# Optimization experiments

Hardware: AMD Instinct MI355X
Metric: run time of the kernel (lower is better)

Reference implementation:

```python
import jax, jax.numpy as jnp
import numpy as np

EPS = 1e-6

def setup_inputs() -> dict:
    key = jax.random.key(0)
    k1, k2 = jax.random.split(key)
    S, B, H, F = 2048, 4, 2048, 8192
    x = jax.random.normal(k1, (S, B, H), dtype=jnp.float32)
    scale = jnp.ones((H,), dtype=jnp.float32)
    ln_bias = jnp.zeros((H,), dtype=jnp.float32)
    kernel = jax.random.normal(k2, (H, F), dtype=jnp.float32) * 0.02  # ~variance_scaling fan_in
    return {"x": x, "scale": scale, "ln_bias": ln_bias, "kernel": kernel}

def reference(x, scale, ln_bias, kernel):
    # LayerNorm over last (hidden) axis, stats in fp32
    mu = jnp.mean(x, axis=-1, keepdims=True)
    var = jnp.mean(jnp.square(x - mu), axis=-1, keepdims=True)
    y = (x - mu) * jax.lax.rsqrt(var + EPS) * scale + ln_bias  # [S,B,H]
    # Dense: contract hidden axis against kernel [H,F]
    z = jnp.einsum('sbh,hf->sbf', y, kernel)  # [S,B,F]
    # return_layernorm_output=True -> (dense_out, ln_out)
    return (z, y)
```

## Files before the change

### kernel.cpp

```cpp
#include <hip/hip_runtime.h>
#include <stdint.h>


typedef __attribute__((ext_vector_type(8))) short short8;
typedef __attribute__((ext_vector_type(4))) float floatx4;

__device__ __forceinline__ unsigned short f2bf(float f) {
    unsigned u = __builtin_bit_cast(unsigned, f);
    u += 0x7fffu + ((u >> 16) & 1u);
    return (unsigned short)(u >> 16);
}

__global__ __launch_bounds__(256) void ln_kernel(
    const float* __restrict__ x, const float* __restrict__ scale,
    const float* __restrict__ bias, float* __restrict__ y,
    unsigned short* __restrict__ ybf, int H)
{
    const int row = blockIdx.x;
    const float* xr = x + (size_t)row * H;
    const int tid = threadIdx.x;

    float4 v0 = ((const float4*)xr)[tid];
    float4 v1 = ((const float4*)xr)[tid + 256];

    float s  = v0.x + v0.y + v0.z + v0.w + v1.x + v1.y + v1.z + v1.w;
    float ss = v0.x*v0.x + v0.y*v0.y + v0.z*v0.z + v0.w*v0.w
             + v1.x*v1.x + v1.y*v1.y + v1.z*v1.z + v1.w*v1.w;

    #pragma unroll
    for (int off = 32; off > 0; off >>= 1) {
        s  += __shfl_down(s,  off, 64);
        ss += __shfl_down(ss, off, 64);
    }
    __shared__ float rs[4], rq[4];
    if ((tid & 63) == 0) { rs[tid >> 6] = s; rq[tid >> 6] = ss; }
    __syncthreads();
    float ts = rs[0] + rs[1] + rs[2] + rs[3];
    float tq = rq[0] + rq[1] + rq[2] + rq[3];
    float mean = ts / (float)H;
    float var  = tq / (float)H - mean * mean;
    float rstd = rsqrtf(var + 1e-6f);

    float4 sc0 = ((const float4*)scale)[tid];
    float4 sc1 = ((const float4*)scale)[tid + 256];
    float4 b0  = ((const float4*)bias)[tid];
    float4 b1  = ((const float4*)bias)[tid + 256];

    float4 o0, o1;
    o0.x = (v0.x - mean) * rstd * sc0.x + b0.x;
    o0.y = (v0.y - mean) * rstd * sc0.y + b0.y;
    o0.z = (v0.z - mean) * rstd * sc0.z + b0.z;
    o0.w = (v0.w - mean) * rstd * sc0.w + b0.w;
    o1.x = (v1.x - mean) * rstd * sc1.x + b1.x;
    o1.y = (v1.y - mean) * rstd * sc1.y + b1.y;
    o1.z = (v1.z - mean) * rstd * sc1.z + b1.z;
    o1.w = (v1.w - mean) * rstd * sc1.w + b1.w;

    float* yr = y + (size_t)row * H;
    ((float4*)yr)[tid]       = o0;
    ((float4*)yr)[tid + 256] = o1;

    unsigned short* br = ybf + (size_t)row * H;
    uint2 p0, p1;
    p0.x = (unsigned)f2bf(o0.x) | ((unsigned)f2bf(o0.y) << 16);
    p0.y = (unsigned)f2bf(o0.z) | ((unsigned)f2bf(o0.w) << 16);
    p1.x = (unsigned)f2bf(o1.x) | ((unsigned)f2bf(o1.y) << 16);
    p1.y = (unsigned)f2bf(o1.z) | ((unsigned)f2bf(o1.w) << 16);
    ((uint2*)br)[tid]       = p0;
    ((uint2*)br)[tid + 256] = p1;
}

__global__ __launch_bounds__(256) void transpose_cast_kernel(
    const float* __restrict__ W, unsigned short* __restrict__ Bt,
    int K, int F)
{
    __shared__ float tile[64][65];
    const int kBase = blockIdx.y * 64;
    const int fBase = blockIdx.x * 64;
    const int tid = threadIdx.x;

    #pragma unroll
    for (int p = 0; p < 4; ++p) {
        int kl = (tid >> 4) + p * 16;
        int fl = (tid & 15) * 4;
        float4 v = *(const float4*)&W[(size_t)(kBase + kl) * F + fBase + fl];
        tile[kl][fl]     = v.x;
        tile[kl][fl + 1] = v.y;
        tile[kl][fl + 2] = v.z;
        tile[kl][fl + 3] = v.w;
    }
    __syncthreads();

    #pragma unroll
    for (int p = 0; p < 2; ++p) {
        int fl = (tid >> 3) + p * 32;
        int k8 = (tid & 7) * 8;
        unsigned w[4];
        #pragma unroll
        for (int j = 0; j < 4; ++j) {
            unsigned lo = f2bf(tile[k8 + 2*j][fl]);
            unsigned hi = f2bf(tile[k8 + 2*j + 1][fl]);
            w[j] = lo | (hi << 16);
        }
        uint4 out = make_uint4(w[0], w[1], w[2], w[3]);
        *(uint4*)&Bt[(size_t)(fBase + fl) * K + kBase + k8] = out;
    }
}

#define BM 128
#define BN 128
#define BK 32

__global__ __launch_bounds__(256) void gemm_bf16_bt(
    const unsigned short* __restrict__ A,
    const unsigned short* __restrict__ Bt,
    float* __restrict__ C,
    int M, int N, int K)
{
    __shared__ unsigned short lsA[BM * BK];
    __shared__ unsigned short lsB[BN * BK];

    const int tid   = threadIdx.x;
    const int lane  = tid & 63;
    const int wave  = tid >> 6;
    const int waveM = wave >> 1;
    const int waveN = wave & 1;
    const int quad  = lane >> 4;
    const int l16   = lane & 15;
    const int qswz  = (quad ^ ((l16 >> 1) & 3)) * 8;

    const int bm = blockIdx.y * BM;
    const int bn = blockIdx.x * BN;

    const unsigned short* gA = A  + (size_t)bm * K;
    const unsigned short* gB = Bt + (size_t)bn * K;

    floatx4 acc[4][4] = {};

    for (int k0 = 0; k0 < K; k0 += BK) {
        __syncthreads();
        #pragma unroll
        for (int i = 0; i < 2; ++i) {
            int e   = i * 256 + tid;
            int row = e >> 2;
            int cs  = (e & 3) ^ ((row >> 1) & 3);
            __builtin_amdgcn_global_load_lds(
                (const __attribute__((address_space(1))) unsigned int*)
                    (gA + (size_t)row * K + k0 + cs * 8),
                (__attribute__((address_space(3))) unsigned int*)
                    (lsA + (size_t)e * 8),
                16, 0, 0);
        }
        #pragma unroll
        for (int i = 0; i < 2; ++i) {
            int e   = i * 256 + tid;
            int row = e >> 2;
            int cs  = (e & 3) ^ ((row >> 1) & 3);
            __builtin_amdgcn_global_load_lds(
                (const __attribute__((address_space(1))) unsigned int*)
                    (gB + (size_t)row * K + k0 + cs * 8),
                (__attribute__((address_space(3))) unsigned int*)
                    (lsB + (size_t)e * 8),
                16, 0, 0);
        }
        __syncthreads();

        short8 a[4], b[4];
        #pragma unroll
        for (int mi = 0; mi < 4; ++mi)
            a[mi] = *(const short8*)&lsA[(waveM*64 + mi*16 + l16) * BK + qswz];
        #pragma unroll
        for (int ni = 0; ni < 4; ++ni)
            b[ni] = *(const short8*)&lsB[(waveN*64 + ni*16 + l16) * BK + qswz];

        #pragma unroll
        for (int mi = 0; mi < 4; ++mi)
            #pragma unroll
            for (int ni = 0; ni < 4; ++ni)
                acc[mi][ni] = __builtin_amdgcn_mfma_f32_16x16x32_bf16(
                    a[mi], b[ni], acc[mi][ni], 0, 0, 0);
    }

    #pragma unroll
    for (int mi = 0; mi < 4; ++mi) {
        #pragma unroll
        for (int ni = 0; ni < 4; ++ni) {
            int col = bn + waveN*64 + ni*16 + l16;
            #pragma unroll
            for (int r = 0; r < 4; ++r) {
                int row = bm + waveM*64 + mi*16 + quad*4 + r;
                C[(size_t)row * N + col] = acc[mi][ni][r];
            }
        }
    }
}

extern "C" void kernel_launch(void* const* d_in, const int* in_sizes, int n_in,
                              void* d_out, int out_size, void* d_ws, size_t ws_size,
                              hipStream_t stream) {
    const float* x      = (const float*)d_in[0];
    const float* scale  = (const float*)d_in[1];
    const float* lnbias = (const float*)d_in[2];
    const float* W      = (const float*)d_in[3];

    const int H = in_sizes[1];
    const int M = in_sizes[0] / H;
    const int F = in_sizes[3] / H;

    float* z = (float*)d_out;
    float* y = z + (size_t)M * F;

    unsigned short* Abf = (unsigned short*)d_ws;
    unsigned short* Btb = Abf + (size_t)M * H;

    ln_kernel<<<M, 256, 0, stream>>>(x, scale, lnbias, y, Abf, H);
    transpose_cast_kernel<<<dim3(F / 64, H / 64), 256, 0, stream>>>(W, Btb, H, F);
    gemm_bf16_bt<<<dim3(F / BN, M / BM), 256, 0, stream>>>(Abf, Btb, z, M, F, H);
}
```

Baseline: 740.8 us.

## Rewrite GEMM with 256x256 tiles, 8 waves, double-buffered LDS and XCD remap

Replaces the 128x128 single-buffered GEMM with a 256x256-tile, 512-thread kernel. It double-buffers LDS in half-K stages so global-to-LDS loads overlap MFMA work, using partial vmcnt waits and raw barriers. It also remaps workgroups across the 8 XCDs for L2 locality and raises MFMA wave priority. This targets low arithmetic intensity and exposed load latency, at the cost of more LDS (128KB per block) and more registers per thread.

```diff
diff --git a/kernel.cpp b/kernel.cpp
--- a/kernel.cpp
+++ b/kernel.cpp
@@ -107,89 +107,140 @@
     }
 }
 
-#define BM 128
-#define BN 128
-#define BK 32
-
-__global__ __launch_bounds__(256) void gemm_bf16_bt(
+#define GBM 256
+#define GBN 256
+#define GBK 64
+
+__device__ __forceinline__ void stage_half(
+    const unsigned short* __restrict__ gA,
+    const unsigned short* __restrict__ gB,
+    unsigned short* dstA,
+    unsigned short* dstB,
+    int t, int kh, int K, int tid)
+{
+    const size_t kb = (size_t)t * GBK + (size_t)kh * 32;
+    #pragma unroll
+    for (int i = 0; i < 2; ++i) {
+        int e  = i * 512 + tid;
+        int r  = e >> 2;
+        int c2 = (e & 3) ^ ((r >> 2) & 3);
+        __builtin_amdgcn_global_load_lds(
+            (const __attribute__((address_space(1))) unsigned int*)
+                (gA + (size_t)r * K + kb + c2 * 8),
+            (__attribute__((address_space(3))) unsigned int*)(dstA + e * 8),
+            16, 0, 0);
+    }
+    #pragma unroll
+    for (int i = 0; i < 2; ++i) {
+        int e  = i * 512 + tid;
+        int r  = e >> 2;
+        int c2 = (e & 3) ^ ((r >> 2) & 3);
+        __builtin_amdgcn_global_load_lds(
+            (const __attribute__((address_space(1))) unsigned int*)
+                (gB + (size_t)r * K + kb + c2 * 8),
+            (__attribute__((address_space(3))) unsigned int*)(dstB + e * 8),
+            16, 0, 0);
+    }
+}
+
+__device__ __forceinline__ void compute_phase(
+    const unsigned short* bufA,
+    const unsigned short* bufB,
+    floatx4 (&acc)[8][4],
+    int waveM, int waveN, int quad, int l16, int sl)
+{
+    short8 a[8], b[4];
+    #pragma unroll
+    for (int mi = 0; mi < 8; ++mi) {
+        int r = waveM * 128 + mi * 16 + l16;
+        a[mi] = *(const short8*)(bufA + ((size_t)r * 4 + sl) * 8);
+    }
+    #pragma unroll
+    for (int ni = 0; ni < 4; ++ni) {
+        int r = waveN * 64 + ni * 16 + l16;
+        b[ni] = *(const short8*)(bufB + ((size_t)r * 4 + sl) * 8);
+    }
+    __builtin_amdgcn_s_setprio(1);
+    #pragma unroll
+    for (int mi = 0; mi < 8; ++mi)
+        #pragma unroll
+        for (int ni = 0; ni < 4; ++ni)
+            acc[mi][ni] = __builtin_amdgcn_mfma_f32_16x16x32_bf16(
+                a[mi], b[ni], acc[mi][ni], 0, 0, 0);
+    __builtin_amdgcn_s_setprio(0);
+}
+
+__global__ __launch_bounds__(512, 2) void gemm_bf16_8w(
     const unsigned short* __restrict__ A,
     const unsigned short* __restrict__ Bt,
     float* __restrict__ C,
     int M, int N, int K)
 {
-    __shared__ unsigned short lsA[BM * BK];
-    __shared__ unsigned short lsB[BN * BK];
+    __shared__ __align__(128) unsigned short lds[2][2][2][8192];
 
     const int tid   = threadIdx.x;
     const int lane  = tid & 63;
     const int wave  = tid >> 6;
-    const int waveM = wave >> 1;
-    const int waveN = wave & 1;
+    const int waveM = wave >> 2;
+    const int waveN = wave & 3;
     const int quad  = lane >> 4;
     const int l16   = lane & 15;
-    const int qswz  = (quad ^ ((l16 >> 1) & 3)) * 8;
-
-    const int bm = blockIdx.y * BM;
-    const int bn = blockIdx.x * BN;
-
-    const unsigned short* gA = A  + (size_t)bm * K;
-    const unsigned short* gB = Bt + (size_t)bn * K;
-
-    floatx4 acc[4][4] = {};
-
-    for (int k0 = 0; k0 < K; k0 += BK) {
-        __syncthreads();
-        #pragma unroll
-        for (int i = 0; i < 2; ++i) {
-            int e   = i * 256 + tid;
-            int row = e >> 2;
-            int cs  = (e & 3) ^ ((row >> 1) & 3);
-            __builtin_amdgcn_global_load_lds(
-                (const __attribute__((address_space(1))) unsigned int*)
-                    (gA + (size_t)row * K + k0 + cs * 8),
-                (__attribute__((address_space(3))) unsigned int*)
-                    (lsA + (size_t)e * 8),
-                16, 0, 0);
-        }
-        #pragma unroll
-        for (int i = 0; i < 2; ++i) {
-            int e   = i * 256 + tid;
-            int row = e >> 2;
-            int cs  = (e & 3) ^ ((row >> 1) & 3);
-            __builtin_amdgcn_global_load_lds(
-                (const __attribute__((address_space(1))) unsigned int*)
-                    (gB + (size_t)row * K + k0 + cs * 8),
-                (__attribute__((address_space(3))) unsigned int*)
-                    (lsB + (size_t)e * 8),
-                16, 0, 0);
-        }
-        __syncthreads();
-
-        short8 a[4], b[4];
-        #pragma unroll
-        for (int mi = 0; mi < 4; ++mi)
-            a[mi] = *(const short8*)&lsA[(waveM*64 + mi*16 + l16) * BK + qswz];
-        #pragma unroll
-        for (int ni = 0; ni < 4; ++ni)
-            b[ni] = *(const short8*)&lsB[(waveN*64 + ni*16 + l16) * BK + qswz];
-
-        #pragma unroll
-        for (int mi = 0; mi < 4; ++mi)
-            #pragma unroll
-            for (int ni = 0; ni < 4; ++ni)
-                acc[mi][ni] = __builtin_amdgcn_mfma_f32_16x16x32_bf16(
-                    a[mi], b[ni], acc[mi][ni], 0, 0, 0);
-    }
-
-    #pragma unroll
-    for (int mi = 0; mi < 4; ++mi) {
+    const int sl    = quad ^ (l16 >> 2);
+
+    const int nwg = gridDim.x;
+    const int cpx = nwg >> 3;
+    const int bid = blockIdx.x;
+    const int wg  = (bid & 7) * cpx + (bid >> 3);
+    const int tilesN = N >> 8;
+    const int tm = wg / tilesN;
+    const int tn = wg % tilesN;
+
+    const unsigned short* gA = A  + (size_t)tm * GBM * K;
+    const unsigned short* gB = Bt + (size_t)tn * GBN * K;
+
+    const int NTt = K >> 6;
+
+    floatx4 acc[8][4] = {};
+
+    stage_half(gA, gB, &lds[0][0][0][0], &lds[0][1][0][0], 0, 0, K, tid);
+    stage_half(gA, gB, &lds[0][0][1][0], &lds[0][1][1][0], 0, 1, K, tid);
+    stage_half(gA, gB, &lds[1][0][0][0], &lds[1][1][0][0], 1, 0, K, tid);
+    asm volatile("s_waitcnt vmcnt(8)" ::: "memory");
+    __builtin_amdgcn_s_barrier();
+
+    for (int t = 0; t < NTt; ++t) {
+        const int p = t & 1;
+        {
+            int ts = (t + 1 < NTt) ? (t + 1) : (NTt - 1);
+            stage_half(gA, gB, &lds[p ^ 1][0][1][0], &lds[p ^ 1][1][1][0],
+                       ts, 1, K, tid);
+            compute_phase(&lds[p][0][0][0], &lds[p][1][0][0], acc,
+                          waveM, waveN, quad, l16, sl);
+            asm volatile("s_waitcnt vmcnt(8)" ::: "memory");
+            __builtin_amdgcn_s_barrier();
+        }
+        {
+            int ts = (t + 2 < NTt) ? (t + 2) : (NTt - 1);
+            stage_half(gA, gB, &lds[p][0][0][0], &lds[p][1][0][0],
+                       ts, 0, K, tid);
+            compute_phase(&lds[p][0][1][0], &lds[p][1][1][0], acc,
+                          waveM, waveN, quad, l16, sl);
+            asm volatile("s_waitcnt vmcnt(8)" ::: "memory");
+            __builtin_amdgcn_s_barrier();
+        }
+    }
+
+    const size_t bm = (size_t)tm * GBM;
+    const size_t bn = (size_t)tn * GBN;
+    #pragma unroll
+    for (int mi = 0; mi < 8; ++mi) {
         #pragma unroll
         for (int ni = 0; ni < 4; ++ni) {
-            int col = bn + waveN*64 + ni*16 + l16;
+            size_t col = bn + (size_t)waveN * 64 + ni * 16 + l16;
             #pragma unroll
             for (int r = 0; r < 4; ++r) {
-                int row = bm + waveM*64 + mi*16 + quad*4 + r;
-                C[(size_t)row * N + col] = acc[mi][ni][r];
+                size_t row = bm + (size_t)waveM * 128 + mi * 16 + quad * 4 + r;
+                C[row * N + col] = acc[mi][ni][r];
             }
         }
     }
@@ -215,5 +266,5 @@
 
     ln_kernel<<<M, 256, 0, stream>>>(x, scale, lnbias, y, Abf, H);
     transpose_cast_kernel<<<dim3(F / 64, H / 64), 256, 0, stream>>>(W, Btb, H, F);
-    gemm_bf16_bt<<<dim3(F / BN, M / BM), 256, 0, stream>>>(Abf, Btb, z, M, F, H);
-}
+    gemm_bf16_8w<<<dim3((M / GBM) * (F / GBN)), 512, 0, stream>>>(Abf, Btb, z, M, F, H);
+}
```

After: 694.0 us. -6.3%, faster.
